# Optimization experiments

Hardware: AMD Instinct MI355X
Metric: run time of the kernel (lower is better)

Reference implementation:

```python
import jax, jax.numpy as jnp
import numpy as np

D_MODEL = 1024
NUM_HEADS = 16
THETA = 10000.0
BATCH = 2
SEQ = 2048


def setup_inputs() -> dict:
    key = jax.random.key(0)
    ks = jax.random.split(key, 5)
    std = (2.0 / (D_MODEL + D_MODEL)) ** 0.5
    mk = lambda k: jax.random.truncated_normal(k, -3.0, 3.0, (D_MODEL, D_MODEL), jnp.float32) * std
    return {
        'x': jax.random.normal(ks[0], (BATCH, SEQ, D_MODEL), jnp.float32),
        'Wq': mk(ks[1]),
        'Wk': mk(ks[2]),
        'Wv': mk(ks[3]),
        'Wo': mk(ks[4]),
        'token_positions': jnp.arange(SEQ, dtype=jnp.int32),
    }


def _apply_rope(x, token_positions, theta):
    # x: (B, H, S, d_k)
    d_k = x.shape[-1]
    freq = 1.0 / theta ** (jnp.arange(0, d_k, 2, dtype=jnp.float32) / d_k)  # (d_k//2,)
    freqs = token_positions.astype(jnp.float32)[:, None] * freq[None, :]   # (S, d_k//2)
    cos, sin = jnp.cos(freqs), jnp.sin(freqs)
    x_real = x[..., 0::2]
    x_imag = x[..., 1::2]
    rot_real = x_real * cos - x_imag * sin
    rot_imag = x_real * sin + x_imag * cos
    # interleave back: (..., d_k//2, 2) -> (..., d_k)
    out = jnp.stack([rot_real, rot_imag], axis=-1)
    return out.reshape(x.shape)


def reference(x, Wq, Wk, Wv, Wo, token_positions):
    B, S, D = x.shape
    H = NUM_HEADS
    d_k = D // H

    def split_heads(t):
        return t.reshape(B, S, H, d_k).transpose(0, 2, 1, 3)  # (B, H, S, d_k)

    Q = split_heads(jnp.einsum('bsd,od->bso', x, Wq))
    K = split_heads(jnp.einsum('bsd,od->bso', x, Wk))
    V = split_heads(jnp.einsum('bsd,od->bso', x, Wv))

    Q = _apply_rope(Q, token_positions, THETA)
    K = _apply_rope(K, token_positions, THETA)

    # naive materialized attention with causal mask, faithful to source
    scores = jnp.einsum('bhqd,bhkd->bhqk', Q, K)
    causal = jnp.tril(jnp.ones((S, S), dtype=bool))  # True = attend
    scores = jnp.where(causal[None, None], scores, -jnp.inf)
    scores = scores / jnp.sqrt(jnp.asarray(d_k, scores.dtype))
    probs = jax.nn.softmax(scores, axis=-1)
    attn = jnp.einsum('bhqk,bhkd->bhqd', probs, V)  # (B, H, S, d_v)

    attn = attn.transpose(0, 2, 1, 3).reshape(B, S, D)
    return jnp.einsum('bsd,od->bso', attn, Wo)
```

## Files before the change

### kernel.cpp

```cpp
#include <hip/hip_runtime.h>
#include <hip/hip_bf16.h>
#include <math.h>

#define NUM_HEADS 16
#define DK 64
#define SEQ 2048
#define BATCHN 2
#define DM 1024
#define BS (BATCHN*SEQ)
#define LSCALE 0.18033688011112042f

typedef __bf16 bf16x8 __attribute__((ext_vector_type(8)));
typedef float floatx4 __attribute__((ext_vector_type(4)));
typedef unsigned short ushort;
typedef unsigned int uint;

__device__ __forceinline__ ushort f2bu(float f){
    union { __hip_bfloat16 h; ushort u; } cv; cv.h = __float2bfloat16(f); return cv.u;
}
__device__ __forceinline__ uint packbf(float a, float b){
    return (uint)f2bu(a) | ((uint)f2bu(b) << 16);
}
__device__ __forceinline__ float bu2f(ushort u){
    union { uint u; float f; } cv; cv.u = (uint)u << 16; return cv.f;
}
__device__ __forceinline__ void gl16(const void* g, void* l){
    __builtin_amdgcn_global_load_lds(
        (const __attribute__((address_space(1))) unsigned int*)g,
        (__attribute__((address_space(3))) unsigned int*)l, 16, 0, 0);
}

__global__ __launch_bounds__(256)
void castall(const float* __restrict__ x,  const float* __restrict__ wq,
             const float* __restrict__ wk, const float* __restrict__ wv,
             const float* __restrict__ wo, const int* __restrict__ pos,
             ushort* __restrict__ xb, ushort* __restrict__ wqkb,
             ushort* __restrict__ wvb, ushort* __restrict__ wob,
             float2* __restrict__ tab)
{
    int bid = blockIdx.x;
    if (bid >= 4096) {
        int idx = (bid - 4096)*256 + threadIdx.x;
        int s = idx >> 5, i = idx & 31;
        float invf = expf(-0.28782313662425575f * (float)i);
        float ang = (float)pos[s] * invf;
        float sn, cs; sincosf(ang, &sn, &cs);
        tab[idx] = make_float2(cs, sn);
        return;
    }
    const float* src; ushort* dst; int off;
    if (bid < 2048)      { src = x;  dst = xb;             off = bid; }
    else if (bid < 2560) { src = wq; dst = wqkb;           off = bid - 2048; }
    else if (bid < 3072) { src = wk; dst = wqkb + 1048576; off = bid - 2560; }
    else if (bid < 3584) { src = wv; dst = wvb;            off = bid - 3072; }
    else                 { src = wo; dst = wob;            off = bid - 3584; }
    int i = off*2048 + threadIdx.x*8;
    float4 a = *(const float4*)(src+i);
    float4 b = *(const float4*)(src+i+4);
    uint4 o;
    o.x = packbf(a.x, a.y);
    o.y = packbf(a.z, a.w);
    o.z = packbf(b.x, b.y);
    o.w = packbf(b.z, b.w);
    *(uint4*)(dst+i) = o;
}

__global__ __launch_bounds__(256)
void proj_fused(const ushort* __restrict__ xb, const ushort* __restrict__ Wqkb,
                const ushort* __restrict__ Wvb, ushort* __restrict__ Qb,
                ushort* __restrict__ VTp, const float2* __restrict__ rope)
{
    __shared__ ushort As[128][32];
    __shared__ ushort Bs[128][32];

    const int bid = blockIdx.x;
    const ushort* A; const ushort* W; int row0, col0, mode;
    if (bid < 512) { A = xb;  W = Wqkb; row0 = (bid >> 4) * 128;
                     col0 = (bid & 15) * 128;  mode = 1; }
    else           { int i = bid - 512; A = Wvb; W = xb;
                     row0 = (i >> 5) * 128; col0 = (i & 31) * 128; mode = 2; }

    const int t = threadIdx.x;
    const int w = t >> 6;
    const int L = t & 63;
    const int lr = L & 15;
    const int lq = L >> 4;
    const int wrow = w * 32;

    floatx4 acc[2][8];
    #pragma unroll
    for (int i = 0; i < 2; ++i)
        #pragma unroll
        for (int j = 0; j < 8; ++j)
            acc[i][j] = (floatx4){0.f,0.f,0.f,0.f};

    const int rr = t >> 2, ko = (t & 3) * 8;
    const ushort* ga = A + (size_t)(row0 + rr) * DM + ko;
    const ushort* gb = W + (size_t)(col0 + rr) * DM + ko;

    for (int k0 = 0; k0 < DM; k0 += 32) {
        __syncthreads();
        gl16(ga + k0,                    &As[rr][ko]);
        gl16(ga + k0 + (size_t)64*DM,    &As[rr + 64][ko]);
        gl16(gb + k0,                    &Bs[rr][ko]);
        gl16(gb + k0 + (size_t)64*DM,    &Bs[rr + 64][ko]);
        __syncthreads();

        bf16x8 aF0 = *(const bf16x8*)&As[wrow + lr][lq*8];
        bf16x8 aF1 = *(const bf16x8*)&As[wrow + 16 + lr][lq*8];
        #pragma unroll
        for (int tc = 0; tc < 8; ++tc) {
            bf16x8 bF = *(const bf16x8*)&Bs[tc*16 + lr][lq*8];
            acc[0][tc] = __builtin_amdgcn_mfma_f32_16x16x32_bf16(aF0, bF, acc[0][tc], 0, 0, 0);
            acc[1][tc] = __builtin_amdgcn_mfma_f32_16x16x32_bf16(aF1, bF, acc[1][tc], 0, 0, 0);
        }
    }

    if (mode == 2) {
        #pragma unroll
        for (int tr = 0; tr < 2; ++tr)
            #pragma unroll
            for (int tc = 0; tc < 8; ++tc)
                #pragma unroll
                for (int r = 0; r < 4; ++r) {
                    int m = row0 + wrow + tr*16 + lq*4 + r;
                    int c = col0 + tc*16 + lr;
                    VTp[(size_t)m * BS + c] = f2bu(acc[tr][tc][r]);
                }
    } else {
        const int mat = col0 >> 10;
        const int base_hh = (col0 & 1023) >> 6;
        ushort* out = Qb + (size_t)mat * (BATCHN*NUM_HEADS*SEQ*DK);
        const float qscale = mat ? 1.f : LSCALE;
        #pragma unroll
        for (int tr = 0; tr < 2; ++tr)
            #pragma unroll
            for (int tc = 0; tc < 8; ++tc)
                #pragma unroll
                for (int r = 0; r < 4; ++r) {
                    int m = row0 + wrow + tr*16 + lq*4 + r;
                    int b = m >> 11;
                    int s = m & (SEQ - 1);
                    int dd = (tc*16 + lr) & 63;
                    int hh = base_hh + (tc >> 2);
                    float v = acc[tr][tc][r];
                    float o = __shfl_xor(v, 1, 64);
                    float2 cs = rope[s*32 + (dd >> 1)];
                    float rv = (dd & 1) ? fmaf(o, cs.y,  v * cs.x)
                                        : fmaf(-o, cs.y, v * cs.x);
                    out[((size_t)((b*NUM_HEADS + hh)*SEQ + s))*DK + dd] =
                        f2bu(rv * qscale);
                }
    }
}

__global__ __launch_bounds__(256)
void gemm_out(const ushort* __restrict__ A, const ushort* __restrict__ W,
              float* __restrict__ out)
{
    __shared__ ushort As[128][32];
    __shared__ ushort Bs[64][32];

    const int t = threadIdx.x;
    const int w = t >> 6;
    const int L = t & 63;
    const int lr = L & 15;
    const int lq = L >> 4;
    const int row0 = blockIdx.y * 128;
    const int col0 = blockIdx.x * 64;
    const int wrow = w * 32;

    floatx4 acc[2][4];
    #pragma unroll
    for (int i = 0; i < 2; ++i)
        #pragma unroll
        for (int j = 0; j < 4; ++j)
            acc[i][j] = (floatx4){0.f,0.f,0.f,0.f};

    const int rr = t >> 2, ko = (t & 3) * 8;
    const ushort* ga = A + (size_t)(row0 + rr) * DM + ko;
    const ushort* gb = W + (size_t)(col0 + rr) * DM + ko;

    for (int k0 = 0; k0 < DM; k0 += 32) {
        __syncthreads();
        gl16(ga + k0,                 &As[rr][ko]);
        gl16(ga + k0 + (size_t)64*DM, &As[rr + 64][ko]);
        gl16(gb + k0,                 &Bs[rr][ko]);
        __syncthreads();

        bf16x8 aF0 = *(const bf16x8*)&As[wrow + lr][lq*8];
        bf16x8 aF1 = *(const bf16x8*)&As[wrow + 16 + lr][lq*8];
        #pragma unroll
        for (int tc = 0; tc < 4; ++tc) {
            bf16x8 bF = *(const bf16x8*)&Bs[tc*16 + lr][lq*8];
            acc[0][tc] = __builtin_amdgcn_mfma_f32_16x16x32_bf16(aF0, bF, acc[0][tc], 0, 0, 0);
            acc[1][tc] = __builtin_amdgcn_mfma_f32_16x16x32_bf16(aF1, bF, acc[1][tc], 0, 0, 0);
        }
    }

    #pragma unroll
    for (int tr = 0; tr < 2; ++tr)
        #pragma unroll
        for (int tc = 0; tc < 4; ++tc)
            #pragma unroll
            for (int r = 0; r < 4; ++r) {
                int m = row0 + wrow + tr*16 + lq*4 + r;
                int c = col0 + tc*16 + lr;
                out[(size_t)m * DM + c] = acc[tr][tc][r];
            }
}

__global__ __launch_bounds__(128)
void attn_mfma(const ushort* __restrict__ Qb, const ushort* __restrict__ Kb,
               const ushort* __restrict__ VT, ushort* __restrict__ attnb,
               ushort* __restrict__ Opart, float* __restrict__ lpart)
{
    __shared__ ushort Ks[64*64];
    __shared__ ushort Vs[64*64];

    const int t = threadIdx.x;
    const int w = t >> 6;
    const int L = t & 63;
    const int lr = L & 15, lq = L >> 4;
    const int h  = blockIdx.y;
    const int b  = blockIdx.z;

    int qt, chunk, nch;
    {
        const int bx = blockIdx.x;
        if (bx < 8)       { qt = bx;              chunk = 0;     nch = 1; }
        else if (bx < 24) { int i = bx - 8;  qt = 8  + (i>>1); chunk = i&1;        nch = 2; }
        else if (bx < 48) { int i = bx - 24; int q3 = i/3; qt = 16 + q3; chunk = i - q3*3; nch = 3; }
        else              { int i = bx - 48; qt = 24 + (i>>2); chunk = i&3;        nch = 4; }
    }
    const int nt = qt + 1;
    const int t0 = (nt * chunk) / nch;
    const int t1 = (nt * (chunk + 1)) / nch;
    const int q0 = qt * 64;
    const int qw = q0 + w * 32;
    const size_t qkbase = (size_t)(b*NUM_HEADS + h) * SEQ * DK;

    bf16x8 qA0, qA1, qB0, qB1;
    {
        const ushort* qp = Qb + qkbase + (size_t)(qw + lr) * DK + lq*8;
        qA0 = *(const bf16x8*)qp;
        qA1 = *(const bf16x8*)(qp + 32);
        qB0 = *(const bf16x8*)(qp + 16*DK);
        qB1 = *(const bf16x8*)(qp + 16*DK + 32);
    }

    floatx4 O0[4], O1[4];
    #pragma unroll
    for (int g = 0; g < 4; ++g) {
        O0[g] = (floatx4){0.f,0.f,0.f,0.f};
        O1[g] = (floatx4){0.f,0.f,0.f,0.f};
    }
    float l0 = 0.f, l1 = 0.f;

    const int sr = t >> 3, t7 = t & 7;
    const int kwb  = (sr*64 + t7*8) ^ ((sr & 7) << 3);
    const int pc0  = ((t7 >> 2) << 3) | ((t7 & 1) << 2) | ((t7 >> 1) & 1);
    const int vwb0 = (sr*64 + pc0*4)     ^ ((sr & 7) << 3);
    const int vwb1 = (sr*64 + pc0*4 + 8) ^ ((sr & 7) << 3);
    const ushort* kpt = Kb + qkbase + (size_t)sr * DK + t7*8;
    const ushort* vpt = VT + ((size_t)(h*DK + sr)) * BS + b*SEQ + t7*8;

    const int kro0 = (lr*64 + lq*8)      ^ ((lr & 7) << 3);
    const int kro1 = (lr*64 + 32 + lq*8) ^ ((lr & 7) << 3);

    for (int tile = t0; tile < t1; ++tile) {
        const int kb = tile * 64;
        const ushort* kg = kpt + (size_t)kb * DK;
        const ushort* vg = vpt + kb;
        uint4 kv0 = *(const uint4*)(kg);
        uint4 kv1 = *(const uint4*)(kg + 16*DK);
        uint4 kv2 = *(const uint4*)(kg + 32*DK);
        uint4 kv3 = *(const uint4*)(kg + 48*DK);
        uint4 vv0 = *(const uint4*)(vg);
        uint4 vv1 = *(const uint4*)(vg + (size_t)16*BS);
        uint4 vv2 = *(const uint4*)(vg + (size_t)32*BS);
        uint4 vv3 = *(const uint4*)(vg + (size_t)48*BS);
        __syncthreads();
        *(uint4*)&Ks[kwb]        = kv0;
        *(uint4*)&Ks[kwb + 1024] = kv1;
        *(uint4*)&Ks[kwb + 2048] = kv2;
        *(uint4*)&Ks[kwb + 3072] = kv3;
        *(uint2*)&Vs[vwb0]        = make_uint2(vv0.x, vv0.y);
        *(uint2*)&Vs[vwb1]        = make_uint2(vv0.z, vv0.w);
        *(uint2*)&Vs[vwb0 + 1024] = make_uint2(vv1.x, vv1.y);
        *(uint2*)&Vs[vwb1 + 1024] = make_uint2(vv1.z, vv1.w);
        *(uint2*)&Vs[vwb0 + 2048] = make_uint2(vv2.x, vv2.y);
        *(uint2*)&Vs[vwb1 + 2048] = make_uint2(vv2.z, vv2.w);
        *(uint2*)&Vs[vwb0 + 3072] = make_uint2(vv3.x, vv3.y);
        *(uint2*)&Vs[vwb1 + 3072] = make_uint2(vv3.z, vv3.w);
        __syncthreads();

        const bool lastt = (tile == nt - 1);
        const int lim0 = qw + lr - kb;
        const int lim1 = lim0 + 16;

        uint2 pk0[4], pk1[4];
        #pragma unroll
        for (int g = 0; g < 4; ++g) {
            bf16x8 kf0 = *(const bf16x8*)&Ks[kro0 + g*1024];
            bf16x8 kf1 = *(const bf16x8*)&Ks[kro1 + g*1024];
            floatx4 s0 = (floatx4){0.f,0.f,0.f,0.f};
            s0 = __builtin_amdgcn_mfma_f32_16x16x32_bf16(kf0, qA0, s0, 0, 0, 0);
            s0 = __builtin_amdgcn_mfma_f32_16x16x32_bf16(kf1, qA1, s0, 0, 0, 0);
            floatx4 s1 = (floatx4){0.f,0.f,0.f,0.f};
            s1 = __builtin_amdgcn_mfma_f32_16x16x32_bf16(kf0, qB0, s1, 0, 0, 0);
            s1 = __builtin_amdgcn_mfma_f32_16x16x32_bf16(kf1, qB1, s1, 0, 0, 0);
            const int kbase = g*16 + lq*4;
            float p0, p1, p2, p3;
            if (lastt) {
                p0 = (kbase + 0 <= lim0) ? exp2f(s0[0]) : 0.f;
                p1 = (kbase + 1 <= lim0) ? exp2f(s0[1]) : 0.f;
                p2 = (kbase + 2 <= lim0) ? exp2f(s0[2]) : 0.f;
                p3 = (kbase + 3 <= lim0) ? exp2f(s0[3]) : 0.f;
            } else {
                p0 = exp2f(s0[0]); p1 = exp2f(s0[1]);
                p2 = exp2f(s0[2]); p3 = exp2f(s0[3]);
            }
            l0 += (p0 + p1) + (p2 + p3);
            pk0[g] = make_uint2(packbf(p0, p1), packbf(p2, p3));
            if (lastt) {
                p0 = (kbase + 0 <= lim1) ? exp2f(s1[0]) : 0.f;
                p1 = (kbase + 1 <= lim1) ? exp2f(s1[1]) : 0.f;
                p2 = (kbase + 2 <= lim1) ? exp2f(s1[2]) : 0.f;
                p3 = (kbase + 3 <= lim1) ? exp2f(s1[3]) : 0.f;
            } else {
                p0 = exp2f(s1[0]); p1 = exp2f(s1[1]);
                p2 = exp2f(s1[2]); p3 = exp2f(s1[3]);
            }
            l1 += (p0 + p1) + (p2 + p3);
            pk1[g] = make_uint2(packbf(p0, p1), packbf(p2, p3));
        }

        #pragma unroll
        for (int c = 0; c < 2; ++c) {
            union { uint u[4]; bf16x8 v; } a0, a1;
            a0.u[0] = pk0[2*c].x;   a0.u[1] = pk0[2*c].y;
            a0.u[2] = pk0[2*c+1].x; a0.u[3] = pk0[2*c+1].y;
            a1.u[0] = pk1[2*c].x;   a1.u[1] = pk1[2*c].y;
            a1.u[2] = pk1[2*c+1].x; a1.u[3] = pk1[2*c+1].y;
            const int vro = c ? kro1 : kro0;
            #pragma unroll
            for (int g2 = 0; g2 < 4; ++g2) {
                bf16x8 vf = *(const bf16x8*)&Vs[vro + g2*1024];
                O0[g2] = __builtin_amdgcn_mfma_f32_16x16x32_bf16(a0.v, vf, O0[g2], 0, 0, 0);
                O1[g2] = __builtin_amdgcn_mfma_f32_16x16x32_bf16(a1.v, vf, O1[g2], 0, 0, 0);
            }
        }
    }

    l0 += __shfl_xor(l0, 16, 64);
    l0 += __shfl_xor(l0, 32, 64);
    l1 += __shfl_xor(l1, 16, 64);
    l1 += __shfl_xor(l1, 32, 64);

    if (nch == 1) {
        #pragma unroll
        for (int r = 0; r < 4; ++r) {
            float li0 = 1.f / __shfl(l0, lq*4 + r, 64);
            float li1 = 1.f / __shfl(l1, lq*4 + r, 64);
            int s0r = qw + lq*4 + r;
            int s1r = qw + 16 + lq*4 + r;
            #pragma unroll
            for (int g2 = 0; g2 < 4; ++g2) {
                attnb[((size_t)(b*SEQ + s0r))*DM + h*DK + g2*16 + lr] = f2bu(O0[g2][r] * li0);
                attnb[((size_t)(b*SEQ + s1r))*DM + h*DK + g2*16 + lr] = f2bu(O1[g2][r] * li1);
            }
        }
    } else {
        const int slot = ((b*NUM_HEADS + h)*24 + (qt - 8))*4 + chunk;
        ushort* Op = Opart + (size_t)slot * 4096;
        #pragma unroll
        for (int r = 0; r < 4; ++r) {
            int ql0 = w*32 + lq*4 + r;
            int ql1 = w*32 + 16 + lq*4 + r;
            #pragma unroll
            for (int g2 = 0; g2 < 4; ++g2) {
                Op[ql0*64 + g2*16 + lr] = f2bu(O0[g2][r]);
                Op[ql1*64 + g2*16 + lr] = f2bu(O1[g2][r]);
            }
        }
        if (lq == 0) {
            lpart[(size_t)slot*64 + w*32 + lr]      = l0;
            lpart[(size_t)slot*64 + w*32 + 16 + lr] = l1;
        }
    }
}

__global__ __launch_bounds__(256)
void combine(const ushort* __restrict__ Opart, const float* __restrict__ lpart,
             ushort* __restrict__ attnb)
{
    int gx = blockIdx.x;
    int qti = gx % 24, bh = gx / 24;
    int h = bh & 15, b = bh >> 4;
    int qt = 8 + qti;
    int nch = (qt >> 3) + 1;
    int tid = threadIdx.x;
    int row = tid >> 2, c0 = (tid & 3) * 16;
    const int base_slot = (bh*24 + qti)*4;

    float acc[16];
    #pragma unroll
    for (int e = 0; e < 16; ++e) acc[e] = 0.f;
    float l = 0.f;

    for (int c = 0; c < nch; ++c) {
        const ushort* Op = Opart + (size_t)(base_slot + c)*4096 + row*64 + c0;
        uint4 u0 = *(const uint4*)(Op);
        uint4 u1 = *(const uint4*)(Op + 8);
        const ushort* h0 = (const ushort*)&u0;
        const ushort* h1 = (const ushort*)&u1;
        #pragma unroll
        for (int e = 0; e < 8; ++e) { acc[e]   += bu2f(h0[e]); }
        #pragma unroll
        for (int e = 0; e < 8; ++e) { acc[8+e] += bu2f(h1[e]); }
        l += lpart[(size_t)(base_slot + c)*64 + row];
    }
    float li = 1.f / l;
    int s = qt*64 + row;
    ushort* dst = attnb + ((size_t)(b*SEQ + s))*DM + h*DK + c0;
    #pragma unroll
    for (int e = 0; e < 16; ++e) dst[e] = f2bu(acc[e] * li);
}

extern "C" void kernel_launch(void* const* d_in, const int* in_sizes, int n_in,
                              void* d_out, int out_size, void* d_ws, size_t ws_size,
                              hipStream_t stream) {
    const float* x   = (const float*)d_in[0];
    const float* Wq  = (const float*)d_in[1];
    const float* Wk  = (const float*)d_in[2];
    const float* Wv  = (const float*)d_in[3];
    const float* Wo  = (const float*)d_in[4];
    const int*   pos = (const int*)d_in[5];
    float* out = (float*)d_out;

    const size_t MB = 1u << 20;
    char* ws = (char*)d_ws;
    ushort* xb    = (ushort*)(ws);
    ushort* Wqkb  = (ushort*)(ws +  8*MB);
    ushort* Wvb   = (ushort*)(ws + 12*MB);
    ushort* Opart = (ushort*)(ws);
    float*  lpart = (float*)(ws + 24*MB);
    ushort* Qb    = (ushort*)(ws + 25*MB);
    ushort* Kb    = (ushort*)(ws + 33*MB);
    ushort* VT    = (ushort*)(ws + 41*MB);
    ushort* attnb = (ushort*)(ws + 49*MB);
    float2* ropeT = (float2*)(ws + 57*MB);
    ushort* Wob   = (ushort*)(ws + 58*MB);

    dim3 blk(256);
    castall<<<4352, blk, 0, stream>>>(x, Wq, Wk, Wv, Wo, pos,
                                      xb, Wqkb, Wvb, Wob, ropeT);

    proj_fused<<<768, blk, 0, stream>>>(xb, Wqkb, Wvb, Qb, VT, ropeT);

    attn_mfma<<<dim3(80, NUM_HEADS, BATCHN), dim3(128), 0, stream>>>(Qb, Kb, VT, attnb,
                                                                     Opart, lpart);
    combine<<<768, blk, 0, stream>>>(Opart, lpart, attnb);

    gemm_out<<<dim3(16,32), blk, 0, stream>>>(attnb, Wob, out);
}
```

Before: 207.2 us.

## Prefetch next K/V tile, peel masked tile, compute row sums via MFMA

The attention loop now issues global loads for the next K/V tile before computing the current one, so load latency overlaps with MFMA work. The causal-mask tile is peeled out of the loop, so the main loop carries no mask branch. Row sums of P are computed with an MFMA against a ones vector, which removes the scalar adds and cross-lane shuffles, and the bf16 pack uses the hardware v_cvt_pk_bf16_f32 and raw exp2 intrinsics. The trade-offs are higher register pressure from holding the prefetch and two extra MFMAs per chunk. The row sums are also now taken from the bf16-rounded probabilities, which slightly changes the normalisation.

```diff
diff --git a/kernel.cpp b/kernel.cpp
--- a/kernel.cpp
+++ b/kernel.cpp
@@ -23,6 +23,10 @@
 }
 __device__ __forceinline__ float bu2f(ushort u){
     union { uint u; float f; } cv; cv.u = (uint)u << 16; return cv.f;
+}
+__device__ __forceinline__ uint cvtpk(float lo, float hi){
+    uint r; asm("v_cvt_pk_bf16_f32 %0, %1, %2" : "=v"(r) : "v"(lo), "v"(hi));
+    return r;
 }
 __device__ __forceinline__ void gl16(const void* g, void* l){
     __builtin_amdgcn_global_load_lds(
@@ -249,13 +253,21 @@
         qB1 = *(const bf16x8*)(qp + 16*DK + 32);
     }
 
+    bf16x8 ones8;
+    {
+        union { uint u[4]; bf16x8 v; } o;
+        o.u[0] = o.u[1] = o.u[2] = o.u[3] = 0x3f803f80u;
+        ones8 = o.v;
+    }
+
     floatx4 O0[4], O1[4];
     #pragma unroll
     for (int g = 0; g < 4; ++g) {
         O0[g] = (floatx4){0.f,0.f,0.f,0.f};
         O1[g] = (floatx4){0.f,0.f,0.f,0.f};
     }
-    float l0 = 0.f, l1 = 0.f;
+    floatx4 lA = (floatx4){0.f,0.f,0.f,0.f};
+    floatx4 lB = (floatx4){0.f,0.f,0.f,0.f};
 
     const int sr = t >> 3, t7 = t & 7;
     const int kwb  = (sr*64 + t7*8) ^ ((sr & 7) << 3);
@@ -268,101 +280,122 @@
     const int kro0 = (lr*64 + lq*8)      ^ ((lr & 7) << 3);
     const int kro1 = (lr*64 + 32 + lq*8) ^ ((lr & 7) << 3);
 
-    for (int tile = t0; tile < t1; ++tile) {
-        const int kb = tile * 64;
-        const ushort* kg = kpt + (size_t)kb * DK;
-        const ushort* vg = vpt + kb;
-        uint4 kv0 = *(const uint4*)(kg);
-        uint4 kv1 = *(const uint4*)(kg + 16*DK);
-        uint4 kv2 = *(const uint4*)(kg + 32*DK);
-        uint4 kv3 = *(const uint4*)(kg + 48*DK);
-        uint4 vv0 = *(const uint4*)(vg);
-        uint4 vv1 = *(const uint4*)(vg + (size_t)16*BS);
-        uint4 vv2 = *(const uint4*)(vg + (size_t)32*BS);
-        uint4 vv3 = *(const uint4*)(vg + (size_t)48*BS);
+    uint4 kv0, kv1, kv2, kv3, vv0, vv1, vv2, vv3;
+
+#define GLOAD(T)                                                              \
+    {                                                                         \
+        const ushort* kg = kpt + (size_t)(T) * 64 * DK;                       \
+        const ushort* vg = vpt + (T) * 64;                                    \
+        kv0 = *(const uint4*)(kg);                                            \
+        kv1 = *(const uint4*)(kg + 16*DK);                                    \
+        kv2 = *(const uint4*)(kg + 32*DK);                                    \
+        kv3 = *(const uint4*)(kg + 48*DK);                                    \
+        vv0 = *(const uint4*)(vg);                                            \
+        vv1 = *(const uint4*)(vg + (size_t)16*BS);                            \
+        vv2 = *(const uint4*)(vg + (size_t)32*BS);                            \
+        vv3 = *(const uint4*)(vg + (size_t)48*BS);                            \
+    }
+
+#define STAGE()                                                               \
+    {                                                                         \
+        *(uint4*)&Ks[kwb]        = kv0;                                       \
+        *(uint4*)&Ks[kwb + 1024] = kv1;                                       \
+        *(uint4*)&Ks[kwb + 2048] = kv2;                                       \
+        *(uint4*)&Ks[kwb + 3072] = kv3;                                       \
+        *(uint2*)&Vs[vwb0]        = make_uint2(vv0.x, vv0.y);                 \
+        *(uint2*)&Vs[vwb1]        = make_uint2(vv0.z, vv0.w);                 \
+        *(uint2*)&Vs[vwb0 + 1024] = make_uint2(vv1.x, vv1.y);                 \
+        *(uint2*)&Vs[vwb1 + 1024] = make_uint2(vv1.z, vv1.w);                 \
+        *(uint2*)&Vs[vwb0 + 2048] = make_uint2(vv2.x, vv2.y);                 \
+        *(uint2*)&Vs[vwb1 + 2048] = make_uint2(vv2.z, vv2.w);                 \
+        *(uint2*)&Vs[vwb0 + 3072] = make_uint2(vv3.x, vv3.y);                 \
+        *(uint2*)&Vs[vwb1 + 3072] = make_uint2(vv3.z, vv3.w);                 \
+    }
+
+#define COMPUTE(LASTT)                                                        \
+    {                                                                         \
+        uint2 pk0[4], pk1[4];                                                 \
+        _Pragma("unroll")                                                     \
+        for (int g = 0; g < 4; ++g) {                                         \
+            bf16x8 kf0 = *(const bf16x8*)&Ks[kro0 + g*1024];                  \
+            bf16x8 kf1 = *(const bf16x8*)&Ks[kro1 + g*1024];                  \
+            floatx4 s0 = (floatx4){0.f,0.f,0.f,0.f};                          \
+            s0 = __builtin_amdgcn_mfma_f32_16x16x32_bf16(kf0, qA0, s0,0,0,0); \
+            s0 = __builtin_amdgcn_mfma_f32_16x16x32_bf16(kf1, qA1, s0,0,0,0); \
+            floatx4 s1 = (floatx4){0.f,0.f,0.f,0.f};                          \
+            s1 = __builtin_amdgcn_mfma_f32_16x16x32_bf16(kf0, qB0, s1,0,0,0); \
+            s1 = __builtin_amdgcn_mfma_f32_16x16x32_bf16(kf1, qB1, s1,0,0,0); \
+            float a0 = __builtin_amdgcn_exp2f(s0[0]);                         \
+            float a1 = __builtin_amdgcn_exp2f(s0[1]);                         \
+            float a2 = __builtin_amdgcn_exp2f(s0[2]);                         \
+            float a3 = __builtin_amdgcn_exp2f(s0[3]);                         \
+            float b0 = __builtin_amdgcn_exp2f(s1[0]);                         \
+            float b1 = __builtin_amdgcn_exp2f(s1[1]);                         \
+            float b2 = __builtin_amdgcn_exp2f(s1[2]);                         \
+            float b3 = __builtin_amdgcn_exp2f(s1[3]);                         \
+            if (LASTT) {                                                      \
+                const int kbase = g*16 + lq*4;                                \
+                a0 = (kbase + 0 <= lim0) ? a0 : 0.f;                          \
+                a1 = (kbase + 1 <= lim0) ? a1 : 0.f;                          \
+                a2 = (kbase + 2 <= lim0) ? a2 : 0.f;                          \
+                a3 = (kbase + 3 <= lim0) ? a3 : 0.f;                          \
+                b0 = (kbase + 0 <= lim1) ? b0 : 0.f;                          \
+                b1 = (kbase + 1 <= lim1) ? b1 : 0.f;                          \
+                b2 = (kbase + 2 <= lim1) ? b2 : 0.f;                          \
+                b3 = (kbase + 3 <= lim1) ? b3 : 0.f;                          \
+            }                                                                 \
+            pk0[g] = make_uint2(cvtpk(a0, a1), cvtpk(a2, a3));                \
+            pk1[g] = make_uint2(cvtpk(b0, b1), cvtpk(b2, b3));                \
+        }                                                                     \
+        _Pragma("unroll")                                                     \
+        for (int c = 0; c < 2; ++c) {                                         \
+            union { uint u[4]; bf16x8 v; } a0u, a1u;                          \
+            a0u.u[0] = pk0[2*c].x;   a0u.u[1] = pk0[2*c].y;                   \
+            a0u.u[2] = pk0[2*c+1].x; a0u.u[3] = pk0[2*c+1].y;                 \
+            a1u.u[0] = pk1[2*c].x;   a1u.u[1] = pk1[2*c].y;                   \
+            a1u.u[2] = pk1[2*c+1].x; a1u.u[3] = pk1[2*c+1].y;                 \
+            lA = __builtin_amdgcn_mfma_f32_16x16x32_bf16(a0u.v, ones8, lA,0,0,0); \
+            lB = __builtin_amdgcn_mfma_f32_16x16x32_bf16(a1u.v, ones8, lB,0,0,0); \
+            const int vro = c ? kro1 : kro0;                                  \
+            _Pragma("unroll")                                                 \
+            for (int g2 = 0; g2 < 4; ++g2) {                                  \
+                bf16x8 vf = *(const bf16x8*)&Vs[vro + g2*1024];               \
+                O0[g2] = __builtin_amdgcn_mfma_f32_16x16x32_bf16(a0u.v, vf, O0[g2],0,0,0); \
+                O1[g2] = __builtin_amdgcn_mfma_f32_16x16x32_bf16(a1u.v, vf, O1[g2],0,0,0); \
+            }                                                                 \
+        }                                                                     \
+    }
+
+    GLOAD(t0);
+    const bool haslast = (t1 == nt);
+    const int tmain = haslast ? t1 - 1 : t1;
+    {
+        const int lim0 = 0, lim1 = 0;
+        for (int tile = t0; tile < tmain; ++tile) {
+            __syncthreads();
+            STAGE();
+            __syncthreads();
+            if (tile + 1 < t1) GLOAD(tile + 1);
+            COMPUTE(false);
+        }
+    }
+    if (haslast) {
         __syncthreads();
-        *(uint4*)&Ks[kwb]        = kv0;
-        *(uint4*)&Ks[kwb + 1024] = kv1;
-        *(uint4*)&Ks[kwb + 2048] = kv2;
-        *(uint4*)&Ks[kwb + 3072] = kv3;
-        *(uint2*)&Vs[vwb0]        = make_uint2(vv0.x, vv0.y);
-        *(uint2*)&Vs[vwb1]        = make_uint2(vv0.z, vv0.w);
-        *(uint2*)&Vs[vwb0 + 1024] = make_uint2(vv1.x, vv1.y);
-        *(uint2*)&Vs[vwb1 + 1024] = make_uint2(vv1.z, vv1.w);
-        *(uint2*)&Vs[vwb0 + 2048] = make_uint2(vv2.x, vv2.y);
-        *(uint2*)&Vs[vwb1 + 2048] = make_uint2(vv2.z, vv2.w);
-        *(uint2*)&Vs[vwb0 + 3072] = make_uint2(vv3.x, vv3.y);
-        *(uint2*)&Vs[vwb1 + 3072] = make_uint2(vv3.z, vv3.w);
+        STAGE();
         __syncthreads();
-
-        const bool lastt = (tile == nt - 1);
-        const int lim0 = qw + lr - kb;
+        const int lim0 = qw + lr - (nt - 1)*64;
         const int lim1 = lim0 + 16;
-
-        uint2 pk0[4], pk1[4];
-        #pragma unroll
-        for (int g = 0; g < 4; ++g) {
-            bf16x8 kf0 = *(const bf16x8*)&Ks[kro0 + g*1024];
-            bf16x8 kf1 = *(const bf16x8*)&Ks[kro1 + g*1024];
-            floatx4 s0 = (floatx4){0.f,0.f,0.f,0.f};
-            s0 = __builtin_amdgcn_mfma_f32_16x16x32_bf16(kf0, qA0, s0, 0, 0, 0);
-            s0 = __builtin_amdgcn_mfma_f32_16x16x32_bf16(kf1, qA1, s0, 0, 0, 0);
-            floatx4 s1 = (floatx4){0.f,0.f,0.f,0.f};
-            s1 = __builtin_amdgcn_mfma_f32_16x16x32_bf16(kf0, qB0, s1, 0, 0, 0);
-            s1 = __builtin_amdgcn_mfma_f32_16x16x32_bf16(kf1, qB1, s1, 0, 0, 0);
-            const int kbase = g*16 + lq*4;
-            float p0, p1, p2, p3;
-            if (lastt) {
-                p0 = (kbase + 0 <= lim0) ? exp2f(s0[0]) : 0.f;
-                p1 = (kbase + 1 <= lim0) ? exp2f(s0[1]) : 0.f;
-                p2 = (kbase + 2 <= lim0) ? exp2f(s0[2]) : 0.f;
-                p3 = (kbase + 3 <= lim0) ? exp2f(s0[3]) : 0.f;
-            } else {
-                p0 = exp2f(s0[0]); p1 = exp2f(s0[1]);
-                p2 = exp2f(s0[2]); p3 = exp2f(s0[3]);
-            }
-            l0 += (p0 + p1) + (p2 + p3);
-            pk0[g] = make_uint2(packbf(p0, p1), packbf(p2, p3));
-            if (lastt) {
-                p0 = (kbase + 0 <= lim1) ? exp2f(s1[0]) : 0.f;
-                p1 = (kbase + 1 <= lim1) ? exp2f(s1[1]) : 0.f;
-                p2 = (kbase + 2 <= lim1) ? exp2f(s1[2]) : 0.f;
-                p3 = (kbase + 3 <= lim1) ? exp2f(s1[3]) : 0.f;
-            } else {
-                p0 = exp2f(s1[0]); p1 = exp2f(s1[1]);
-                p2 = exp2f(s1[2]); p3 = exp2f(s1[3]);
-            }
-            l1 += (p0 + p1) + (p2 + p3);
-            pk1[g] = make_uint2(packbf(p0, p1), packbf(p2, p3));
-        }
-
-        #pragma unroll
-        for (int c = 0; c < 2; ++c) {
-            union { uint u[4]; bf16x8 v; } a0, a1;
-            a0.u[0] = pk0[2*c].x;   a0.u[1] = pk0[2*c].y;
-            a0.u[2] = pk0[2*c+1].x; a0.u[3] = pk0[2*c+1].y;
-            a1.u[0] = pk1[2*c].x;   a1.u[1] = pk1[2*c].y;
-            a1.u[2] = pk1[2*c+1].x; a1.u[3] = pk1[2*c+1].y;
-            const int vro = c ? kro1 : kro0;
-            #pragma unroll
-            for (int g2 = 0; g2 < 4; ++g2) {
-                bf16x8 vf = *(const bf16x8*)&Vs[vro + g2*1024];
-                O0[g2] = __builtin_amdgcn_mfma_f32_16x16x32_bf16(a0.v, vf, O0[g2], 0, 0, 0);
-                O1[g2] = __builtin_amdgcn_mfma_f32_16x16x32_bf16(a1.v, vf, O1[g2], 0, 0, 0);
-            }
-        }
-    }
-
-    l0 += __shfl_xor(l0, 16, 64);
-    l0 += __shfl_xor(l0, 32, 64);
-    l1 += __shfl_xor(l1, 16, 64);
-    l1 += __shfl_xor(l1, 32, 64);
+        COMPUTE(true);
+    }
+#undef GLOAD
+#undef STAGE
+#undef COMPUTE
 
     if (nch == 1) {
         #pragma unroll
         for (int r = 0; r < 4; ++r) {
-            float li0 = 1.f / __shfl(l0, lq*4 + r, 64);
-            float li1 = 1.f / __shfl(l1, lq*4 + r, 64);
+            float li0 = 1.f / lA[r];
+            float li1 = 1.f / lB[r];
             int s0r = qw + lq*4 + r;
             int s1r = qw + 16 + lq*4 + r;
             #pragma unroll
@@ -384,9 +417,12 @@
                 Op[ql1*64 + g2*16 + lr] = f2bu(O1[g2][r]);
             }
         }
-        if (lq == 0) {
-            lpart[(size_t)slot*64 + w*32 + lr]      = l0;
-            lpart[(size_t)slot*64 + w*32 + 16 + lr] = l1;
+        if (lr == 0) {
+            #pragma unroll
+            for (int r = 0; r < 4; ++r) {
+                lpart[(size_t)slot*64 + w*32 + lq*4 + r]      = lA[r];
+                lpart[(size_t)slot*64 + w*32 + 16 + lq*4 + r] = lB[r];
+            }
         }
     }
 }
```

Result: faster. 189.8 us (-8.4%).
